# Optimization experiments

Measured on AMD Instinct MI355X. Metric: run time of the kernel, lower is better.

The kernel has to match this reference:

```python
import jax, jax.numpy as jnp
import numpy as np

EMBED_DIM = 1024
NUM_HEADS = 16
HEAD_DIM = EMBED_DIM // NUM_HEADS
SPARSITY_LAMBDA = 0.01
B, S = 2, 2048


def setup_inputs() -> dict:
    key = jax.random.key(0)
    ks = jax.random.split(key, 10)
    scale = 0.02
    inp = {
        "x": jax.random.normal(ks[0], (B, S, EMBED_DIM), dtype=jnp.float32),
        "Wq": jax.random.normal(ks[1], (EMBED_DIM, EMBED_DIM), dtype=jnp.float32) * scale,
        "bq": jnp.zeros((EMBED_DIM,), dtype=jnp.float32),
        "Wk": jax.random.normal(ks[2], (EMBED_DIM, EMBED_DIM), dtype=jnp.float32) * scale,
        "bk": jnp.zeros((EMBED_DIM,), dtype=jnp.float32),
        "Wv": jax.random.normal(ks[3], (EMBED_DIM, EMBED_DIM), dtype=jnp.float32) * scale,
        "bv": jnp.zeros((EMBED_DIM,), dtype=jnp.float32),
        "Wo": jax.random.normal(ks[4], (EMBED_DIM, EMBED_DIM), dtype=jnp.float32) * scale,
        "bo": jnp.zeros((EMBED_DIM,), dtype=jnp.float32),
        "z": jax.random.normal(ks[5], (NUM_HEADS,), dtype=jnp.float32),
    }
    return inp


def reference(x, Wq, bq, Wk, bk, Wv, bv, Wo, bo, z):
    # Linear layers (torch Linear: y = x @ W.T + b); W here stored as [out, in]
    def split_heads(t):  # [B,S,E] -> [B,H,S,D]
        return t.reshape(B, S, NUM_HEADS, HEAD_DIM).transpose(0, 2, 1, 3)

    q = split_heads(x @ Wq.T + bq)
    k = split_heads(x @ Wk.T + bk)
    v = split_heads(x @ Wv.T + bv)

    scores = jnp.einsum("bhsd,bhtd->bhst", q, k) / jnp.sqrt(jnp.float32(HEAD_DIM))
    gate = jax.nn.sigmoid(z)  # [H], per-head scalar gate on raw scores
    scores = scores * gate[None, :, None, None]
    probs = jax.nn.softmax(scores, axis=-1)
    ctx = jnp.einsum("bhst,bhtd->bhsd", probs, v)  # [B,H,S,D]
    ctx = ctx.transpose(0, 2, 1, 3).reshape(B, S, EMBED_DIM)
    out = ctx @ Wo.T + bo
    penalty = jnp.sum(jax.nn.sigmoid(z)) * SPARSITY_LAMBDA
    return out, penalty
```

## Files before the change

kernel.cpp:

```cpp
#include <hip/hip_runtime.h>

typedef unsigned short ushort_t;
typedef __bf16 bf16x8 __attribute__((ext_vector_type(8)));
typedef ushort_t u16x8 __attribute__((ext_vector_type(8)));
typedef float f32x4 __attribute__((ext_vector_type(4)));

#define DEVI __device__ __forceinline__

constexpr int Ed = 1024;
constexpr int Hh = 16;
constexpr int Dd = 64;
constexpr int Ss = 2048;
constexpr int Mm = 4096;

constexpr int NX4 = Mm * Ed / 4;
constexpr int NW4 = Ed * Ed / 4;

DEVI ushort_t f2bf(float f) {
    union { float f; unsigned int i; } v; v.f = f;
    unsigned int r = v.i + 0x7fffu + ((v.i >> 16) & 1u);
    return (ushort_t)(r >> 16);
}

__global__ __launch_bounds__(256) void cvt_all(
    const float* __restrict__ x,  const float* __restrict__ Wq,
    const float* __restrict__ Wk, const float* __restrict__ Wv,
    const float* __restrict__ Wo,
    ushort_t* __restrict__ xb,  ushort_t* __restrict__ Wqb,
    ushort_t* __restrict__ Wkb, ushort_t* __restrict__ Wvb,
    ushort_t* __restrict__ Wob)
{
    int i = blockIdx.x * 256 + threadIdx.x;
    const float* s; ushort_t* d; int off;
    if (i < NX4)                { s = x;  d = xb;  off = i; }
    else if (i < NX4 + NW4)     { s = Wq; d = Wqb; off = i - NX4; }
    else if (i < NX4 + 2 * NW4) { s = Wk; d = Wkb; off = i - NX4 - NW4; }
    else if (i < NX4 + 3 * NW4) { s = Wv; d = Wvb; off = i - NX4 - 2 * NW4; }
    else                        { s = Wo; d = Wob; off = i - NX4 - 3 * NW4; }
    float4 v = ((const float4*)s)[off];
    ushort4 o; o.x = f2bf(v.x); o.y = f2bf(v.y); o.z = f2bf(v.z); o.w = f2bf(v.w);
    ((ushort4*)d)[off] = o;
}

DEVI void gld16(const void* g, void* l) {
    __builtin_amdgcn_global_load_lds(
        (__attribute__((address_space(1))) void*)(g),
        (__attribute__((address_space(3))) void*)(l), 16, 0, 0);
}

DEVI void gemm_core(const ushort_t* __restrict__ A, const ushort_t* __restrict__ W,
                    ushort_t* As, ushort_t* Bs, int tm, int tn, int K,
                    f32x4 acc[4][4])
{
    const int tid  = threadIdx.x;
    const int w    = tid >> 6;
    const int lane = tid & 63;
    const int quad = lane >> 4;
    const int l15  = lane & 15;
    const int wy   = w >> 1, wx = w & 1;
    const int rowc = lane >> 3;
    const int col8 = (lane & 7) * 8;

    for (int k0 = 0; k0 < K; k0 += 64) {
        __syncthreads();
#pragma unroll
        for (int i = 0; i < 4; ++i) {
            int chunk = w * 4 + i;
            int row = chunk * 8 + rowc;
            gld16(A + (size_t)(tm + row) * K + k0 + col8, (char*)As + chunk * 1024);
            gld16(W + (size_t)(tn + row) * K + k0 + col8, (char*)Bs + chunk * 1024);
        }
        __syncthreads();
#pragma unroll
        for (int ks = 0; ks < 64; ks += 32) {
            bf16x8 a[4], b[4];
#pragma unroll
            for (int mi = 0; mi < 4; ++mi)
                a[mi] = *(const bf16x8*)&As[(wy * 64 + mi * 16 + l15) * 64 + ks + quad * 8];
#pragma unroll
            for (int ni = 0; ni < 4; ++ni)
                b[ni] = *(const bf16x8*)&Bs[(wx * 64 + ni * 16 + l15) * 64 + ks + quad * 8];
#pragma unroll
            for (int mi = 0; mi < 4; ++mi)
#pragma unroll
                for (int ni = 0; ni < 4; ++ni)
                    acc[mi][ni] = __builtin_amdgcn_mfma_f32_16x16x32_bf16(
                        a[mi], b[ni], acc[mi][ni], 0, 0, 0);
        }
    }
}

__global__ __launch_bounds__(256, 2) void qkv_gemm(
    const ushort_t* __restrict__ x,
    const ushort_t* __restrict__ Wq, const float* __restrict__ bq,
    const ushort_t* __restrict__ Wk, const float* __restrict__ bk,
    const ushort_t* __restrict__ Wv, const float* __restrict__ bv,
    ushort_t* __restrict__ qo, ushort_t* __restrict__ ko, ushort_t* __restrict__ vto)
{
    __shared__ __align__(16) ushort_t As[128 * 64];
    __shared__ __align__(16) ushort_t Bs[128 * 64];
    const ushort_t* W; const float* bias; ushort_t* outp; int vmode;
    if (blockIdx.z == 0)      { W = Wq; bias = bq; outp = qo;  vmode = 0; }
    else if (blockIdx.z == 1) { W = Wk; bias = bk; outp = ko;  vmode = 0; }
    else                      { W = Wv; bias = bv; outp = vto; vmode = 1; }

    const int tm = blockIdx.x * 128, tn = blockIdx.y * 128;
    f32x4 acc[4][4] = {};
    gemm_core(x, W, As, Bs, tm, tn, Ed, acc);

    const int tid = threadIdx.x, w = tid >> 6, lane = tid & 63;
    const int quad = lane >> 4, l15 = lane & 15;
    const int wy = w >> 1, wx = w & 1;
#pragma unroll
    for (int ni = 0; ni < 4; ++ni) {
        int gc = tn + wx * 64 + ni * 16 + l15;
        float bb = bias[gc];
        int h = gc >> 6, d = gc & 63;
#pragma unroll
        for (int mi = 0; mi < 4; ++mi) {
#pragma unroll
            for (int r = 0; r < 4; ++r) {
                int gr = tm + wy * 64 + mi * 16 + quad * 4 + r;
                int b_ = gr >> 11, s_ = gr & 2047;
                float v = acc[mi][ni][r] + bb;
                size_t addr;
                if (vmode == 0) addr = ((size_t)(b_ * Hh + h) * Ss + s_) * Dd + d;
                else            addr = ((size_t)(b_ * Hh + h) * Dd + d) * Ss + s_;
                outp[addr] = f2bf(v);
            }
        }
    }
}

__global__ __launch_bounds__(256, 2) void out_gemm(
    const ushort_t* __restrict__ ctx, const ushort_t* __restrict__ Wo,
    const float* __restrict__ bo, float* __restrict__ out)
{
    __shared__ __align__(16) ushort_t As[128 * 64];
    __shared__ __align__(16) ushort_t Bs[128 * 64];
    const int tm = blockIdx.x * 128, tn = blockIdx.y * 128;
    f32x4 acc[4][4] = {};
    gemm_core(ctx, Wo, As, Bs, tm, tn, Ed, acc);

    const int tid = threadIdx.x, w = tid >> 6, lane = tid & 63;
    const int quad = lane >> 4, l15 = lane & 15;
    const int wy = w >> 1, wx = w & 1;
#pragma unroll
    for (int ni = 0; ni < 4; ++ni) {
        int gc = tn + wx * 64 + ni * 16 + l15;
        float bb = bo[gc];
#pragma unroll
        for (int mi = 0; mi < 4; ++mi)
#pragma unroll
            for (int r = 0; r < 4; ++r) {
                int gr = tm + wy * 64 + mi * 16 + quad * 4 + r;
                out[(size_t)gr * Ed + gc] = acc[mi][ni][r] + bb;
            }
    }
}

__global__ __launch_bounds__(256, 6) void attn(
    const ushort_t* __restrict__ Q, const ushort_t* __restrict__ Kk,
    const ushort_t* __restrict__ Vt, const float* __restrict__ z,
    ushort_t* __restrict__ ctx)
{
    __shared__ __align__(16) ushort_t Ks[64 * 68];
    __shared__ __align__(16) ushort_t Vs[64 * 68];
    __shared__ __align__(16) ushort_t Ps[4][16 * 68];

    const int tid = threadIdx.x, w = tid >> 6, lane = tid & 63;
    const int quad = lane >> 4, l15 = lane & 15;
    const int qt = blockIdx.x;
    const int bh = blockIdx.y;
    const int h = bh & (Hh - 1), b_ = bh >> 4;
    const size_t base = (size_t)bh * Ss * Dd;

    const float gate = 1.f / (1.f + __expf(-z[h]));
    const float scl2 = gate * 0.125f * 1.44269504f;

    bf16x8 aQ[2];
#pragma unroll
    for (int c = 0; c < 2; ++c)
        aQ[c] = *(const bf16x8*)&Q[base + (size_t)(qt * 64 + w * 16 + l15) * Dd
                                   + c * 32 + quad * 8];

    f32x4 accO[4] = {};
    float lsum[4] = {0.f, 0.f, 0.f, 0.f};

    for (int kt = 0; kt < Ss / 64; ++kt) {
        __syncthreads();
#pragma unroll
        for (int i = 0; i < 2; ++i) {
            int e8  = tid + i * 256;
            int row = e8 >> 3;
            int c8  = (e8 & 7) * 8;
            *(u16x8*)&Ks[row * 68 + c8] =
                *(const u16x8*)&Kk[base + (size_t)(kt * 64 + row) * Dd + c8];
            *(u16x8*)&Vs[row * 68 + c8] =
                *(const u16x8*)&Vt[base + (size_t)row * Ss + kt * 64 + c8];
        }
        __syncthreads();

        f32x4 sAcc[4] = {};
#pragma unroll
        for (int ni = 0; ni < 4; ++ni) {
            bf16x8 b0 = *(const bf16x8*)&Ks[(ni * 16 + l15) * 68 + quad * 8];
            bf16x8 b1 = *(const bf16x8*)&Ks[(ni * 16 + l15) * 68 + 32 + quad * 8];
            sAcc[ni] = __builtin_amdgcn_mfma_f32_16x16x32_bf16(aQ[0], b0, sAcc[ni], 0, 0, 0);
            sAcc[ni] = __builtin_amdgcn_mfma_f32_16x16x32_bf16(aQ[1], b1, sAcc[ni], 0, 0, 0);
        }

#pragma unroll
        for (int ni = 0; ni < 4; ++ni)
#pragma unroll
            for (int r = 0; r < 4; ++r) {
                float p = exp2f(sAcc[ni][r] * scl2);
                lsum[r] += p;
                Ps[w][(quad * 4 + r) * 68 + ni * 16 + l15] = f2bf(p);
            }

#pragma unroll
        for (int c = 0; c < 2; ++c) {
            bf16x8 aP = *(const bf16x8*)&Ps[w][l15 * 68 + c * 32 + quad * 8];
#pragma unroll
            for (int ni = 0; ni < 4; ++ni) {
                bf16x8 bV = *(const bf16x8*)&Vs[(ni * 16 + l15) * 68 + c * 32 + quad * 8];
                accO[ni] = __builtin_amdgcn_mfma_f32_16x16x32_bf16(aP, bV, accO[ni], 0, 0, 0);
            }
        }
    }

#pragma unroll
    for (int r = 0; r < 4; ++r) {
        lsum[r] += __shfl_xor(lsum[r], 1);
        lsum[r] += __shfl_xor(lsum[r], 2);
        lsum[r] += __shfl_xor(lsum[r], 4);
        lsum[r] += __shfl_xor(lsum[r], 8);
    }

#pragma unroll
    for (int r = 0; r < 4; ++r) {
        int srow = qt * 64 + w * 16 + quad * 4 + r;
        float inv = 1.f / lsum[r];
#pragma unroll
        for (int ni = 0; ni < 4; ++ni) {
            int d = ni * 16 + l15;
            ctx[((size_t)(b_ * Ss + srow)) * Ed + h * Dd + d] = f2bf(accO[ni][r] * inv);
        }
    }
}

__global__ void penalty_k(const float* __restrict__ z, float* __restrict__ out) {
    if (threadIdx.x == 0) {
        float s = 0.f;
        for (int h = 0; h < Hh; ++h) s += 1.f / (1.f + __expf(-z[h]));
        out[(size_t)Mm * Ed] = s * 0.01f;
    }
}

extern "C" void kernel_launch(void* const* d_in, const int* in_sizes, int n_in,
                              void* d_out, int out_size, void* d_ws, size_t ws_size,
                              hipStream_t stream) {
    const float* x  = (const float*)d_in[0];
    const float* Wq = (const float*)d_in[1];
    const float* bq = (const float*)d_in[2];
    const float* Wk = (const float*)d_in[3];
    const float* bk = (const float*)d_in[4];
    const float* Wv = (const float*)d_in[5];
    const float* bv = (const float*)d_in[6];
    const float* Wo = (const float*)d_in[7];
    const float* bo = (const float*)d_in[8];
    const float* z  = (const float*)d_in[9];
    float* out = (float*)d_out;

    ushort_t* xb  = (ushort_t*)d_ws;
    ushort_t* Wqb = xb  + (size_t)Mm * Ed;
    ushort_t* Wkb = Wqb + (size_t)Ed * Ed;
    ushort_t* Wvb = Wkb + (size_t)Ed * Ed;
    ushort_t* Wob = Wvb + (size_t)Ed * Ed;
    ushort_t* qw  = Wob + (size_t)Ed * Ed;
    ushort_t* kw  = qw + (size_t)Mm * Ed;
    ushort_t* vT  = kw + (size_t)Mm * Ed;
    ushort_t* cx  = vT + (size_t)Mm * Ed;

    dim3 blk(256);
    cvt_all<<<dim3((NX4 + 4 * NW4) / 256), blk, 0, stream>>>(
        x, Wq, Wk, Wv, Wo, xb, Wqb, Wkb, Wvb, Wob);
    qkv_gemm<<<dim3(Mm / 128, Ed / 128, 3), blk, 0, stream>>>(
        xb, Wqb, bq, Wkb, bk, Wvb, bv, qw, kw, vT);
    attn<<<dim3(Ss / 64, 2 * Hh), blk, 0, stream>>>(qw, kw, vT, z, cx);
    out_gemm<<<dim3(Mm / 128, Ed / 128), blk, 0, stream>>>(cx, Wob, bo, out);
    penalty_k<<<1, 64, 0, stream>>>(z, out);
}
```

Before: 246.5 us.

## Load attention K/V tiles directly global-to-LDS with XOR swizzle instead of padding

The attention kernel's K and V tile loads now go straight from global memory into LDS through the gld16 helper, instead of being staged through registers. The padded 68-stride shared layout becomes an unpadded 64-stride layout with an XOR swizzle on 16-byte chunks, applied on the source address at load time and on the read offsets for the MFMA operands, to avoid bank conflicts. The launch-bounds occupancy hint is also lowered from 6 to 4 blocks. The aim is to cut load-issue instructions and VGPR pressure; the lower occupancy hint could reduce latency hiding.

```diff
diff --git a/kernel.cpp b/kernel.cpp
--- a/kernel.cpp
+++ b/kernel.cpp
@@ -159,13 +159,13 @@
     }
 }
 
-__global__ __launch_bounds__(256, 6) void attn(
+__global__ __launch_bounds__(256, 4) void attn(
     const ushort_t* __restrict__ Q, const ushort_t* __restrict__ Kk,
     const ushort_t* __restrict__ Vt, const float* __restrict__ z,
     ushort_t* __restrict__ ctx)
 {
-    __shared__ __align__(16) ushort_t Ks[64 * 68];
-    __shared__ __align__(16) ushort_t Vs[64 * 68];
+    __shared__ __align__(16) ushort_t Ks[64 * 64];
+    __shared__ __align__(16) ushort_t Vs[64 * 64];
     __shared__ __align__(16) ushort_t Ps[4][16 * 68];
 
     const int tid = threadIdx.x, w = tid >> 6, lane = tid & 63;
@@ -184,28 +184,37 @@
         aQ[c] = *(const bf16x8*)&Q[base + (size_t)(qt * 64 + w * 16 + l15) * Dd
                                    + c * 32 + quad * 8];
 
+    const int rowA = w * 16 + (lane >> 3);
+    const int rowB = rowA + 8;
+    const int gsA  = (lane & 7) ^ (rowA & 7);
+    const int gsB  = (lane & 7) ^ (rowB & 7);
+    const ushort_t* kSrcA = Kk + base + (size_t)rowA * Dd + gsA * 8;
+    const ushort_t* kSrcB = Kk + base + (size_t)rowB * Dd + gsB * 8;
+    const ushort_t* vSrcA = Vt + base + (size_t)rowA * Ss + gsA * 8;
+    const ushort_t* vSrcB = Vt + base + (size_t)rowB * Ss + gsB * 8;
+    ushort_t* kDstA = Ks + (w * 2) * 512;
+    ushort_t* kDstB = Ks + (w * 2 + 1) * 512;
+    ushort_t* vDstA = Vs + (w * 2) * 512;
+    ushort_t* vDstB = Vs + (w * 2 + 1) * 512;
+
     f32x4 accO[4] = {};
     float lsum[4] = {0.f, 0.f, 0.f, 0.f};
 
+    const int swq = (l15 & 7) * 8;
+
     for (int kt = 0; kt < Ss / 64; ++kt) {
         __syncthreads();
-#pragma unroll
-        for (int i = 0; i < 2; ++i) {
-            int e8  = tid + i * 256;
-            int row = e8 >> 3;
-            int c8  = (e8 & 7) * 8;
-            *(u16x8*)&Ks[row * 68 + c8] =
-                *(const u16x8*)&Kk[base + (size_t)(kt * 64 + row) * Dd + c8];
-            *(u16x8*)&Vs[row * 68 + c8] =
-                *(const u16x8*)&Vt[base + (size_t)row * Ss + kt * 64 + c8];
-        }
+        gld16(kSrcA + (size_t)kt * 64 * Dd, kDstA);
+        gld16(kSrcB + (size_t)kt * 64 * Dd, kDstB);
+        gld16(vSrcA + kt * 64, vDstA);
+        gld16(vSrcB + kt * 64, vDstB);
         __syncthreads();
 
         f32x4 sAcc[4] = {};
 #pragma unroll
         for (int ni = 0; ni < 4; ++ni) {
-            bf16x8 b0 = *(const bf16x8*)&Ks[(ni * 16 + l15) * 68 + quad * 8];
-            bf16x8 b1 = *(const bf16x8*)&Ks[(ni * 16 + l15) * 68 + 32 + quad * 8];
+            bf16x8 b0 = *(const bf16x8*)&Ks[(ni * 16 + l15) * 64 + ((quad ^ 0) * 8 ^ swq)];
+            bf16x8 b1 = *(const bf16x8*)&Ks[(ni * 16 + l15) * 64 + ((quad + 4) * 8 ^ swq)];
             sAcc[ni] = __builtin_amdgcn_mfma_f32_16x16x32_bf16(aQ[0], b0, sAcc[ni], 0, 0, 0);
             sAcc[ni] = __builtin_amdgcn_mfma_f32_16x16x32_bf16(aQ[1], b1, sAcc[ni], 0, 0, 0);
         }
@@ -224,7 +233,7 @@
             bf16x8 aP = *(const bf16x8*)&Ps[w][l15 * 68 + c * 32 + quad * 8];
 #pragma unroll
             for (int ni = 0; ni < 4; ++ni) {
-                bf16x8 bV = *(const bf16x8*)&Vs[(ni * 16 + l15) * 68 + c * 32 + quad * 8];
+                bf16x8 bV = *(const bf16x8*)&Vs[(ni * 16 + l15) * 64 + (((quad + 4 * c) * 8) ^ swq)];
                 accO[ni] = __builtin_amdgcn_mfma_f32_16x16x32_bf16(aP, bV, accO[ni], 0, 0, 0);
             }
         }
```

New measurement: 230.9 us. 1.07x faster.
